# Optimization experiments

Measured on AMD Instinct MI355X. Metric: run time of the kernel, lower is better.

## Reference

```python
import jax, jax.numpy as jnp
import numpy as np

B, N, C = 8, 4096, 512
H = W = 64           # N = H * W, dimensionality == 2
SHIFT = 4            # shift_size
WS = 8               # window_size
R = 4                # mlp_ratio
EPS = 1e-6


def setup_inputs() -> dict:
    key = jax.random.key(0)
    ks = jax.random.split(key, 3)
    return {
        "inputs": jax.random.normal(ks[0], (B, N, C), dtype=jnp.float32),
        # second_norm (LayerNormalization) params
        "ln_gamma": jnp.ones((C,), jnp.float32),
        "ln_beta": jnp.zeros((C,), jnp.float32),
        # MLP params: Dense(C*R) -> gelu -> Dense(C)
        "W1": jax.random.normal(ks[1], (C, C * R), dtype=jnp.float32) * 0.02,
        "b1": jnp.zeros((C * R,), jnp.float32),
        "W2": jax.random.normal(ks[2], (C * R, C), dtype=jnp.float32) * 0.02,
        "b2": jnp.zeros((C,), jnp.float32),
    }


def _layer_norm(x, gamma, beta):
    mu = jnp.mean(x, axis=-1, keepdims=True)
    var = jnp.mean(jnp.square(x - mu), axis=-1, keepdims=True)
    return (x - mu) * jax.lax.rsqrt(var + EPS) * gamma + beta


def reference(inputs, ln_gamma, ln_beta, W1, b1, W2, b2):
    # NOTE: faithful to the provided call(): first_norm and attention are
    # never invoked (`normed = x`, `self_att = windowed`), so the window
    # partition + reverse is an exact identity round-trip of the shifted grid.
    grid = inputs.reshape(B, H, W, C)
    shifted = jnp.roll(grid, (-SHIFT, -SHIFT), axis=(1, 2))  # SwinCyclicShifter

    # window partition: [B, nH, nW, WS, WS, C] windows of WSxWS patches
    nh = H // WS
    win = shifted.reshape(B, nh, WS, nh, WS, C).transpose(0, 1, 3, 2, 4, 5)
    # (identity "attention" on [B*nH*nW, WS*WS, C]) then window reverse
    unwin = win.transpose(0, 1, 3, 2, 4, 5).reshape(B, N, C)

    x = unwin + inputs                       # residual add
    normed = _layer_norm(x, ln_gamma, ln_beta)
    h = jax.nn.gelu(normed @ W1 + b1)        # [B, N, 4C]
    mlp_out = h @ W2 + b2                    # [B, N, C]
    return mlp_out + x
```

## Files before the change

kernel.cpp:

```cpp
#include <hip/hip_runtime.h>
#include <hip/hip_bf16.h>
#include <cstdint>
#include <cstddef>


typedef short bf16x8 __attribute__((ext_vector_type(8)));
typedef float f32x4 __attribute__((ext_vector_type(4)));

#define GLOBAL_AS(p) ((__attribute__((address_space(1))) void*)(uintptr_t)(p))
#define LDS_AS(p)    ((__attribute__((address_space(3))) void*)(p))

static __device__ __forceinline__ ushort f2bf(float f) {
    uint32_t u = __float_as_uint(f);
    uint32_t r = (u + 0x7FFFu + ((u >> 16) & 1u)) >> 16;
    return (ushort)r;
}

static __device__ __forceinline__ float gelu_e2(float v) {
    float v2 = v * v;
    float m = fmaf(-0.1029433f, v2, -2.3022084f);
    float t = v * m;
    float e;
    asm("v_exp_f32 %0, %1" : "=v"(e) : "v"(t));
    return v * __builtin_amdgcn_rcpf(1.0f + e);
}

static __device__ __forceinline__ int rolled_row(int row) {
    int b = row >> 12, n = row & 4095;
    int h = n >> 6, wv = n & 63;
    int n2 = (((h + 4) & 63) << 6) | ((wv + 4) & 63);
    return (b << 12) | n2;
}

#define SBAR() do { __builtin_amdgcn_sched_barrier(0); \
                    __builtin_amdgcn_s_barrier(); \
                    __builtin_amdgcn_sched_barrier(0); } while (0)

#define LBAR() do { __builtin_amdgcn_sched_barrier(0); \
                    asm volatile("s_waitcnt lgkmcnt(0)" ::: "memory"); \
                    __builtin_amdgcn_s_barrier(); \
                    __builtin_amdgcn_sched_barrier(0); } while (0)

__global__ __launch_bounds__(256)
void prep_kernel(const float* __restrict__ in, const float* __restrict__ gamma,
                 const float* __restrict__ beta, ushort* __restrict__ normed,
                 const float* __restrict__ W1, ushort* __restrict__ W1T,
                 const float* __restrict__ W2, ushort* __restrict__ W2T) {
    const int bid = blockIdx.x;
    if (bid < 16384) {
        const int half = threadIdx.x >> 7;
        const int t = threadIdx.x & 127;
        const int wave = threadIdx.x >> 6;
        const int row = bid * 2 + half;
        const int row2 = rolled_row(row);

        const float4* p0 = (const float4*)(in + (size_t)row * 512);
        const float4* p1 = (const float4*)(in + (size_t)row2 * 512);
        float4 a = p0[t], c = p1[t];
        float x0 = a.x + c.x, x1 = a.y + c.y, x2 = a.z + c.z, x3 = a.w + c.w;

        float s = x0 + x1 + x2 + x3;
        float sq = x0 * x0 + x1 * x1 + x2 * x2 + x3 * x3;
#pragma unroll
        for (int o = 32; o > 0; o >>= 1) {
            s += __shfl_xor(s, o);
            sq += __shfl_xor(sq, o);
        }
        __shared__ float red[4][2];
        if ((threadIdx.x & 63) == 0) { red[wave][0] = s; red[wave][1] = sq; }
        __syncthreads();
        const int w0 = half * 2;
        s = red[w0][0] + red[w0 + 1][0];
        sq = red[w0][1] + red[w0 + 1][1];
        float mu = s * (1.0f / 512.0f);
        float var = sq * (1.0f / 512.0f) - mu * mu;
        float rs = rsqrtf(var + 1e-6f);

        float4 g = ((const float4*)gamma)[t];
        float4 be = ((const float4*)beta)[t];
        ushort4 o4;
        o4.x = f2bf((x0 - mu) * rs * g.x + be.x);
        o4.y = f2bf((x1 - mu) * rs * g.y + be.y);
        o4.z = f2bf((x2 - mu) * rs * g.z + be.z);
        o4.w = f2bf((x3 - mu) * rs * g.w + be.w);
        ((ushort4*)(normed + (size_t)row * 512))[t] = o4;
    } else {
        __shared__ float tile[32][33];
        const int tx = threadIdx.x & 31, ty = threadIdx.x >> 5;
        const bool isW2 = bid >= 17408;
        const int i = isW2 ? (bid - 17408) : (bid - 16384);
        const int NBX = isW2 ? 16 : 64;
        const int Ccols = isW2 ? 512 : 2048;
        const int R = isW2 ? 2048 : 512;
        const float* src = isW2 ? W2 : W1;
        ushort* dst = isW2 ? W2T : W1T;
        const int bx = (i % NBX) * 32;
        const int by = (i / NBX) * 32;
#pragma unroll
        for (int r = 0; r < 32; r += 8)
            tile[ty + r][tx] = src[(size_t)(by + ty + r) * Ccols + bx + tx];
        __syncthreads();
        int k = by + tx;
        int kd = isW2 ? ((k & ~63) | ((k & 15) << 2) | ((k >> 4) & 3)) : k;
#pragma unroll
        for (int r = 0; r < 32; r += 8)
            dst[(size_t)(bx + ty + r) * R + kd] = f2bf(tile[tx][ty + r]);
    }
}

__global__ __launch_bounds__(256, 4)
void mlp_gemm1(const ushort* __restrict__ A, const ushort* __restrict__ Bt,
               const float* __restrict__ bias, ushort* __restrict__ outH) {
    constexpr int K = 512, N = 2048, BK = 64;
    __shared__ ushort Asm[128 * BK];
    __shared__ ushort Bsm[128 * BK];

    const int t = threadIdx.x;
    const int w = t >> 6, l = t & 63;
    const int wr = w >> 1, wc = w & 1;

    const int bid = blockIdx.x;
    const int xcd = bid & 7, idx = bid >> 3;
    const int brow = ((xcd << 5) + (idx >> 4)) << 7;
    const int bcol = (idx & 15) << 7;

    f32x4 acc[4][4] = {};

    const int trow = t >> 3;
    const int csrc = (((t & 7) ^ ((t >> 3) & 7)) << 3);
    const size_t aBase = (size_t)(brow + trow) * K + csrc;
    const size_t bBase = (size_t)(bcol + trow) * K + csrc;
    char* const ldsA = (char*)Asm + w * 1024;
    char* const ldsB = (char*)Bsm + w * 1024;

    const int rA = l & 15;
    const int cb0 = ((l >> 4) ^ (rA & 7)) << 4;
    const int bA0 = (wr << 13) + (rA << 7) + cb0;
    const int bB0 = (wc << 13) + (rA << 7) + cb0;
    const char* const pA0 = (const char*)Asm + bA0;
    const char* const pA1 = (const char*)Asm + (bA0 ^ 64);
    const char* const pB0 = (const char*)Bsm + bB0;
    const char* const pB1 = (const char*)Bsm + (bB0 ^ 64);

    for (int k0 = 0; k0 < K; k0 += BK) {
#pragma unroll
        for (int i = 0; i < 4; ++i) {
            __builtin_amdgcn_global_load_lds(GLOBAL_AS(A + aBase + (size_t)(i * 32) * K + k0),
                                             LDS_AS(ldsA + i * 4096), 16, 0, 0);
            __builtin_amdgcn_global_load_lds(GLOBAL_AS(Bt + bBase + (size_t)(i * 32) * K + k0),
                                             LDS_AS(ldsB + i * 4096), 16, 0, 0);
        }
        __syncthreads();

#pragma unroll
        for (int s = 0; s < 2; ++s) {
            const char* pa = s ? pA1 : pA0;
            const char* pb = s ? pB1 : pB0;
            bf16x8 aF[4], bF[4];
#pragma unroll
            for (int i = 0; i < 4; ++i)
                aF[i] = *(const bf16x8*)(pa + i * 2048);
#pragma unroll
            for (int j = 0; j < 4; ++j)
                bF[j] = *(const bf16x8*)(pb + j * 2048);
#pragma unroll
            for (int i = 0; i < 4; ++i)
#pragma unroll
                for (int j = 0; j < 4; ++j)
                    acc[i][j] = __builtin_amdgcn_mfma_f32_16x16x32_bf16(aF[i], bF[j], acc[i][j], 0, 0, 0);
        }
        __syncthreads();
    }

    const int cm = (l >> 4) << 2;
    const int cn = l & 15;
    float bvv[4];
#pragma unroll
    for (int j = 0; j < 4; ++j)
        bvv[j] = bias[bcol + wc * 64 + j * 16 + cn];
    const int ecol = bcol + wc * 64 + (cn << 2);
#pragma unroll
    for (int i = 0; i < 4; ++i) {
#pragma unroll
        for (int r = 0; r < 4; ++r) {
            const int row = brow + wr * 64 + i * 16 + cm + r;
            float f0 = gelu_e2(acc[i][0][r] + bvv[0]);
            float f1 = gelu_e2(acc[i][1][r] + bvv[1]);
            float f2 = gelu_e2(acc[i][2][r] + bvv[2]);
            float f3 = gelu_e2(acc[i][3][r] + bvv[3]);
            uint32_t lo, hi;
            asm("v_cvt_pk_bf16_f32 %0, %1, %2" : "=v"(lo) : "v"(f0), "v"(f1));
            asm("v_cvt_pk_bf16_f32 %0, %1, %2" : "=v"(hi) : "v"(f2), "v"(f3));
            uint2 pv; pv.x = lo; pv.y = hi;
            *(uint2*)(outH + (size_t)row * N + ecol) = pv;
        }
    }
}

__global__ __launch_bounds__(512, 2)
void mlp_gemm2(const ushort* __restrict__ A, const ushort* __restrict__ Bt,
               const float* __restrict__ bias, const float* __restrict__ resid,
               float* __restrict__ outF) {
    constexpr int KT = 2048, TT = 32, N = 512;
    __shared__ __align__(16) char sm[131072];
    const int t = threadIdx.x;
    const int w = t >> 6, l = t & 63;
    const int wr = w >> 2, wc = w & 3;

    const int nwg = gridDim.x;
    const int bid = blockIdx.x;
    const int swz = (bid & 7) * (nwg >> 3) + (bid >> 3);
    const int cb = swz & 1;
    const int rgrp = swz >> 1;
    const int brow0 = rgrp * 256;
    const int bcol = cb << 8;

    const int kksw = (((t & 3) ^ ((t >> 3) & 3)) << 3);
    const size_t aTh = (size_t)(t >> 2) * KT + kksw;
    const size_t bTh = (size_t)(bcol + (t >> 2)) * KT + kksw;
    const ushort* const aPanel = A + (size_t)brow0 * KT;
    char* const dA = (char*)sm + (w << 10);
    char* const dB = dA + 65536;

    const int xorv = ((l >> 1) & 3) << 4;
    const int preA = ((((wr << 7) + (l & 15)) << 6) + ((l >> 4) << 4)) ^ xorv;
    const int preB = 65536 + (((((wc << 6) + (l & 15)) << 6) + ((l >> 4) << 4)) ^ xorv);

    f32x4 acc[8][4] = {};
    bf16x8 aF[4], bF[4];

    auto issueA = [&](int T, int kh) {
        const int slot = ((T & 1) << 1) | kh;
        const ushort* s = aPanel + aTh + T * 64 + kh * 32;
        char* d = dA + (slot << 14);
        __builtin_amdgcn_global_load_lds(GLOBAL_AS(s), LDS_AS(d), 16, 0, 0);
        __builtin_amdgcn_global_load_lds(GLOBAL_AS(s + (size_t)128 * KT), LDS_AS(d + 8192), 16, 0, 0);
    };
    auto issueB = [&](int T, int kh) {
        const int slot = ((T & 1) << 1) | kh;
        const ushort* s = Bt + bTh + T * 64 + kh * 32;
        char* d = dB + (slot << 14);
        __builtin_amdgcn_global_load_lds(GLOBAL_AS(s), LDS_AS(d), 16, 0, 0);
        __builtin_amdgcn_global_load_lds(GLOBAL_AS(s + (size_t)128 * KT), LDS_AS(d + 8192), 16, 0, 0);
    };
    auto rdA = [&](int slot, int mb) {
        const char* p = (const char*)sm + (slot << 14) + preA + (mb << 12);
        aF[0] = *(const bf16x8*)(p);
        aF[1] = *(const bf16x8*)(p + 1024);
        aF[2] = *(const bf16x8*)(p + 2048);
        aF[3] = *(const bf16x8*)(p + 3072);
    };
    auto rdB = [&](int slot) {
        const char* p = (const char*)sm + (slot << 14) + preB;
        bF[0] = *(const bf16x8*)(p);
        bF[1] = *(const bf16x8*)(p + 1024);
        bF[2] = *(const bf16x8*)(p + 2048);
        bF[3] = *(const bf16x8*)(p + 3072);
    };
    auto mfma16 = [&](int mb) {
        __builtin_amdgcn_s_setprio(1);
#pragma unroll
        for (int mf = 0; mf < 4; ++mf)
#pragma unroll
            for (int nf = 0; nf < 4; ++nf)
                acc[mb * 4 + mf][nf] = __builtin_amdgcn_mfma_f32_16x16x32_bf16(
                    aF[mf], bF[nf], acc[mb * 4 + mf][nf], 0, 0, 0);
        __builtin_amdgcn_s_setprio(0);
    };

    auto tile_body = [&](int T) {
        const int s0 = (T & 1) << 1;
        rdA(s0, 0); rdB(s0);
        if (T + 1 < TT) issueB(T + 1, 1);
        SBAR();
        mfma16(0);
        SBAR();
        rdA(s0, 1);
        if (T + 2 < TT) issueA(T + 2, 0);
        SBAR();
        mfma16(1);
        SBAR();
        rdA(s0 + 1, 0); rdB(s0 + 1);
        if (T + 2 < TT) issueB(T + 2, 0);
        SBAR();
        mfma16(0);
        SBAR();
        rdA(s0 + 1, 1);
        if (T + 2 < TT) issueA(T + 2, 1);
        SBAR();
        mfma16(1);
        __builtin_amdgcn_sched_barrier(0);
        if (T < TT - 2)       { asm volatile("s_waitcnt vmcnt(6)" ::: "memory"); }
        else if (T == TT - 2) { asm volatile("s_waitcnt vmcnt(0)" ::: "memory"); }
        SBAR();
    };

    issueA(0, 0); issueB(0, 0);
    issueA(0, 1); issueB(0, 1);
    issueA(1, 0); issueB(1, 0);
    issueA(1, 1);
    __builtin_amdgcn_sched_barrier(0);
    asm volatile("s_waitcnt vmcnt(6)" ::: "memory");
    SBAR();

#pragma unroll 1
    for (int T = 0; T < TT; ++T)
        tile_body(T);

#pragma unroll
    for (int h2 = 0; h2 < 2; ++h2) {
        if (wr == h2) {
#pragma unroll
            for (int mf = 0; mf < 8; ++mf)
#pragma unroll
                for (int nf = 0; nf < 4; ++nf)
#pragma unroll
                    for (int r = 0; r < 4; ++r) {
                        int rl = mf * 16 + ((l >> 4) << 2) + r;
                        int col = (wc << 6) + nf * 16 + (l & 15);
                        *(float*)(sm + rl * 1024 + col * 4) = acc[mf][nf][r];
                    }
        }
        LBAR();
#pragma unroll
        for (int k = 0; k < 16; ++k) {
            int c = t + (k << 9);
            int row = c >> 6, c4 = c & 63;
            f32x4 v = *(const f32x4*)(sm + ((size_t)c << 4));
            int R = brow0 + (h2 << 7) + row;
            int col0 = bcol + (c4 << 2);
            f32x4 bb = *(const f32x4*)(bias + col0);
            f32x4 x0 = *(const f32x4*)(resid + (size_t)R * 512 + col0);
            f32x4 x1 = *(const f32x4*)(resid + (size_t)rolled_row(R) * 512 + col0);
            v = v + bb + x0 + x1;
            *(f32x4*)(outF + (size_t)R * N + col0) = v;
        }
        if (h2 == 0) LBAR();
    }
}

extern "C" void kernel_launch(void* const* d_in, const int* in_sizes, int n_in,
                              void* d_out, int out_size, void* d_ws, size_t ws_size,
                              hipStream_t stream) {
    const float* in = (const float*)d_in[0];
    const float* ln_g = (const float*)d_in[1];
    const float* ln_b = (const float*)d_in[2];
    const float* W1 = (const float*)d_in[3];
    const float* b1 = (const float*)d_in[4];
    const float* W2 = (const float*)d_in[5];
    const float* b2 = (const float*)d_in[6];
    float* out = (float*)d_out;

    char* ws = (char*)d_ws;
    ushort* normed = (ushort*)ws;
    ushort* hbuf   = (ushort*)(ws + (size_t)32 * 1024 * 1024);
    ushort* W1T    = (ushort*)(ws + (size_t)160 * 1024 * 1024);
    ushort* W2T    = (ushort*)(ws + (size_t)162 * 1024 * 1024);

    prep_kernel<<<dim3(18432), 256, 0, stream>>>(in, ln_g, ln_b, normed,
                                                 W1, W1T, W2, W2T);
    mlp_gemm1<<<dim3(4096), 256, 0, stream>>>(normed, W1T, b1, hbuf);
    mlp_gemm2<<<dim3(256), 512, 0, stream>>>(hbuf, W2T, b2, in, out);
}
```

Baseline: 192.1 us.

## Replace pipelined 256x256 GEMM2 with simpler 128x128 tile kernel at higher occupancy

Rewrites the second MLP GEMM from a 512-thread, 256x256-tile kernel with a hand-scheduled double-buffered LDS pipeline into a 256-thread, 128x128-tile kernel with a single LDS buffer and plain syncthreads. More, smaller workgroups (1024 instead of 256) with up to 4 per CU are meant to hide latency through occupancy rather than explicit prefetch. The epilogue now writes directly from registers with scalar stores instead of staging through LDS for coalesced vector stores. This gives up operand reuse, load/compute overlap and store coalescing.

```diff
diff --git a/kernel.cpp b/kernel.cpp
--- a/kernel.cpp
+++ b/kernel.cpp
@@ -31,15 +31,6 @@
     int n2 = (((h + 4) & 63) << 6) | ((wv + 4) & 63);
     return (b << 12) | n2;
 }
-
-#define SBAR() do { __builtin_amdgcn_sched_barrier(0); \
-                    __builtin_amdgcn_s_barrier(); \
-                    __builtin_amdgcn_sched_barrier(0); } while (0)
-
-#define LBAR() do { __builtin_amdgcn_sched_barrier(0); \
-                    asm volatile("s_waitcnt lgkmcnt(0)" ::: "memory"); \
-                    __builtin_amdgcn_s_barrier(); \
-                    __builtin_amdgcn_sched_barrier(0); } while (0)
 
 __global__ __launch_bounds__(256)
 void prep_kernel(const float* __restrict__ in, const float* __restrict__ gamma,
@@ -197,145 +188,90 @@
     }
 }
 
-__global__ __launch_bounds__(512, 2)
+__global__ __launch_bounds__(256, 4)
 void mlp_gemm2(const ushort* __restrict__ A, const ushort* __restrict__ Bt,
                const float* __restrict__ bias, const float* __restrict__ resid,
                float* __restrict__ outF) {
-    constexpr int KT = 2048, TT = 32, N = 512;
-    __shared__ __align__(16) char sm[131072];
+    constexpr int K = 2048, N = 512, BK = 64;
+    __shared__ ushort Asm[128 * BK];
+    __shared__ ushort Bsm[128 * BK];
+
     const int t = threadIdx.x;
     const int w = t >> 6, l = t & 63;
-    const int wr = w >> 2, wc = w & 3;
-
-    const int nwg = gridDim.x;
+    const int wr = w >> 1, wc = w & 1;
+
     const int bid = blockIdx.x;
-    const int swz = (bid & 7) * (nwg >> 3) + (bid >> 3);
-    const int cb = swz & 1;
-    const int rgrp = swz >> 1;
-    const int brow0 = rgrp * 256;
-    const int bcol = cb << 8;
-
-    const int kksw = (((t & 3) ^ ((t >> 3) & 3)) << 3);
-    const size_t aTh = (size_t)(t >> 2) * KT + kksw;
-    const size_t bTh = (size_t)(bcol + (t >> 2)) * KT + kksw;
-    const ushort* const aPanel = A + (size_t)brow0 * KT;
-    char* const dA = (char*)sm + (w << 10);
-    char* const dB = dA + 65536;
-
-    const int xorv = ((l >> 1) & 3) << 4;
-    const int preA = ((((wr << 7) + (l & 15)) << 6) + ((l >> 4) << 4)) ^ xorv;
-    const int preB = 65536 + (((((wc << 6) + (l & 15)) << 6) + ((l >> 4) << 4)) ^ xorv);
-
-    f32x4 acc[8][4] = {};
-    bf16x8 aF[4], bF[4];
-
-    auto issueA = [&](int T, int kh) {
-        const int slot = ((T & 1) << 1) | kh;
-        const ushort* s = aPanel + aTh + T * 64 + kh * 32;
-        char* d = dA + (slot << 14);
-        __builtin_amdgcn_global_load_lds(GLOBAL_AS(s), LDS_AS(d), 16, 0, 0);
-        __builtin_amdgcn_global_load_lds(GLOBAL_AS(s + (size_t)128 * KT), LDS_AS(d + 8192), 16, 0, 0);
-    };
-    auto issueB = [&](int T, int kh) {
-        const int slot = ((T & 1) << 1) | kh;
-        const ushort* s = Bt + bTh + T * 64 + kh * 32;
-        char* d = dB + (slot << 14);
-        __builtin_amdgcn_global_load_lds(GLOBAL_AS(s), LDS_AS(d), 16, 0, 0);
-        __builtin_amdgcn_global_load_lds(GLOBAL_AS(s + (size_t)128 * KT), LDS_AS(d + 8192), 16, 0, 0);
-    };
-    auto rdA = [&](int slot, int mb) {
-        const char* p = (const char*)sm + (slot << 14) + preA + (mb << 12);
-        aF[0] = *(const bf16x8*)(p);
-        aF[1] = *(const bf16x8*)(p + 1024);
-        aF[2] = *(const bf16x8*)(p + 2048);
-        aF[3] = *(const bf16x8*)(p + 3072);
-    };
-    auto rdB = [&](int slot) {
-        const char* p = (const char*)sm + (slot << 14) + preB;
-        bF[0] = *(const bf16x8*)(p);
-        bF[1] = *(const bf16x8*)(p + 1024);
-        bF[2] = *(const bf16x8*)(p + 2048);
-        bF[3] = *(const bf16x8*)(p + 3072);
-    };
-    auto mfma16 = [&](int mb) {
-        __builtin_amdgcn_s_setprio(1);
-#pragma unroll
-        for (int mf = 0; mf < 4; ++mf)
-#pragma unroll
-            for (int nf = 0; nf < 4; ++nf)
-                acc[mb * 4 + mf][nf] = __builtin_amdgcn_mfma_f32_16x16x32_bf16(
-                    aF[mf], bF[nf], acc[mb * 4 + mf][nf], 0, 0, 0);
-        __builtin_amdgcn_s_setprio(0);
-    };
-
-    auto tile_body = [&](int T) {
-        const int s0 = (T & 1) << 1;
-        rdA(s0, 0); rdB(s0);
-        if (T + 1 < TT) issueB(T + 1, 1);
-        SBAR();
-        mfma16(0);
-        SBAR();
-        rdA(s0, 1);
-        if (T + 2 < TT) issueA(T + 2, 0);
-        SBAR();
-        mfma16(1);
-        SBAR();
-        rdA(s0 + 1, 0); rdB(s0 + 1);
-        if (T + 2 < TT) issueB(T + 2, 0);
-        SBAR();
-        mfma16(0);
-        SBAR();
-        rdA(s0 + 1, 1);
-        if (T + 2 < TT) issueA(T + 2, 1);
-        SBAR();
-        mfma16(1);
-        __builtin_amdgcn_sched_barrier(0);
-        if (T < TT - 2)       { asm volatile("s_waitcnt vmcnt(6)" ::: "memory"); }
-        else if (T == TT - 2) { asm volatile("s_waitcnt vmcnt(0)" ::: "memory"); }
-        SBAR();
-    };
-
-    issueA(0, 0); issueB(0, 0);
-    issueA(0, 1); issueB(0, 1);
-    issueA(1, 0); issueB(1, 0);
-    issueA(1, 1);
-    __builtin_amdgcn_sched_barrier(0);
-    asm volatile("s_waitcnt vmcnt(6)" ::: "memory");
-    SBAR();
-
-#pragma unroll 1
-    for (int T = 0; T < TT; ++T)
-        tile_body(T);
-
-#pragma unroll
-    for (int h2 = 0; h2 < 2; ++h2) {
-        if (wr == h2) {
-#pragma unroll
-            for (int mf = 0; mf < 8; ++mf)
-#pragma unroll
-                for (int nf = 0; nf < 4; ++nf)
-#pragma unroll
-                    for (int r = 0; r < 4; ++r) {
-                        int rl = mf * 16 + ((l >> 4) << 2) + r;
-                        int col = (wc << 6) + nf * 16 + (l & 15);
-                        *(float*)(sm + rl * 1024 + col * 4) = acc[mf][nf][r];
-                    }
-        }
-        LBAR();
-#pragma unroll
-        for (int k = 0; k < 16; ++k) {
-            int c = t + (k << 9);
-            int row = c >> 6, c4 = c & 63;
-            f32x4 v = *(const f32x4*)(sm + ((size_t)c << 4));
-            int R = brow0 + (h2 << 7) + row;
-            int col0 = bcol + (c4 << 2);
-            f32x4 bb = *(const f32x4*)(bias + col0);
-            f32x4 x0 = *(const f32x4*)(resid + (size_t)R * 512 + col0);
-            f32x4 x1 = *(const f32x4*)(resid + (size_t)rolled_row(R) * 512 + col0);
-            v = v + bb + x0 + x1;
-            *(f32x4*)(outF + (size_t)R * N + col0) = v;
-        }
-        if (h2 == 0) LBAR();
+    const int xcd = bid & 7, idx = bid >> 3;
+    const int brow = ((xcd << 5) + (idx >> 2)) << 7;
+    const int bcol = (idx & 3) << 7;
+
+    f32x4 acc[4][4] = {};
+
+    const int trow = t >> 3;
+    const int csrc = (((t & 7) ^ ((t >> 3) & 7)) << 3);
+    const size_t aBase = (size_t)(brow + trow) * K + csrc;
+    const size_t bBase = (size_t)(bcol + trow) * K + csrc;
+    char* const ldsA = (char*)Asm + w * 1024;
+    char* const ldsB = (char*)Bsm + w * 1024;
+
+    const int rA = l & 15;
+    const int cb0 = ((l >> 4) ^ (rA & 7)) << 4;
+    const int bA0 = (wr << 13) + (rA << 7) + cb0;
+    const int bB0 = (wc << 13) + (rA << 7) + cb0;
+    const char* const pA0 = (const char*)Asm + bA0;
+    const char* const pA1 = (const char*)Asm + (bA0 ^ 64);
+    const char* const pB0 = (const char*)Bsm + bB0;
+    const char* const pB1 = (const char*)Bsm + (bB0 ^ 64);
+
+    for (int k0 = 0; k0 < K; k0 += BK) {
+#pragma unroll
+        for (int i = 0; i < 4; ++i) {
+            __builtin_amdgcn_global_load_lds(GLOBAL_AS(A + aBase + (size_t)(i * 32) * K + k0),
+                                             LDS_AS(ldsA + i * 4096), 16, 0, 0);
+            __builtin_amdgcn_global_load_lds(GLOBAL_AS(Bt + bBase + (size_t)(i * 32) * K + k0),
+                                             LDS_AS(ldsB + i * 4096), 16, 0, 0);
+        }
+        __syncthreads();
+
+#pragma unroll
+        for (int s = 0; s < 2; ++s) {
+            const char* pa = s ? pA1 : pA0;
+            const char* pb = s ? pB1 : pB0;
+            bf16x8 aF[4], bF[4];
+#pragma unroll
+            for (int i = 0; i < 4; ++i)
+                aF[i] = *(const bf16x8*)(pa + i * 2048);
+#pragma unroll
+            for (int j = 0; j < 4; ++j)
+                bF[j] = *(const bf16x8*)(pb + j * 2048);
+#pragma unroll
+            for (int i = 0; i < 4; ++i)
+#pragma unroll
+                for (int j = 0; j < 4; ++j)
+                    acc[i][j] = __builtin_amdgcn_mfma_f32_16x16x32_bf16(aF[i], bF[j], acc[i][j], 0, 0, 0);
+        }
+        __syncthreads();
+    }
+
+    const int cm = (l >> 4) << 2;
+    const int cn = l & 15;
+    float bvv[4];
+#pragma unroll
+    for (int j = 0; j < 4; ++j)
+        bvv[j] = bias[bcol + wc * 64 + j * 16 + cn];
+#pragma unroll
+    for (int i = 0; i < 4; ++i) {
+#pragma unroll
+        for (int r = 0; r < 4; ++r) {
+            const int row = brow + wr * 64 + i * 16 + cm + r;
+            const float* x0 = resid + (size_t)row * 512;
+            const float* x1 = resid + (size_t)rolled_row(row) * 512;
+#pragma unroll
+            for (int j = 0; j < 4; ++j) {
+                const int col = bcol + wc * 64 + j * 16 + cn;
+                outF[(size_t)row * N + col] = acc[i][j][r] + bvv[j] + x0[col] + x1[col];
+            }
+        }
     }
 }
 
@@ -360,5 +296,5 @@
     prep_kernel<<<dim3(18432), 256, 0, stream>>>(in, ln_g, ln_b, normed,
                                                  W1, W1T, W2, W2T);
     mlp_gemm1<<<dim3(4096), 256, 0, stream>>>(normed, W1T, b1, hbuf);
-    mlp_gemm2<<<dim3(256), 512, 0, stream>>>(hbuf, W2T, b2, in, out);
-}
+    mlp_gemm2<<<dim3(1024), 256, 0, stream>>>(hbuf, W2T, b2, in, out);
+}
```

After: 189.1 us. About the same (-1.5%).
